# Kernel tuning notes

Measured on AMD Instinct MI355X. Metric: run time of the kernel, lower is better.

## Reference

```python
import jax, jax.numpy as jnp
import numpy as np

B, LG = 16, 128            # graphs, nodes per graph
N = B * LG                 # total nodes
LAT, HID, EE, NL = 32, 128, 32, 3
T_STEPS = 100


def setup_inputs() -> dict:
    key = jax.random.key(0)
    ks = list(jax.random.split(key, 64))
    ki = iter(ks)

    def gl(shape):
        fan_in = shape[-2] if len(shape) >= 2 else shape[-1]
        return jax.random.normal(next(ki), shape, dtype=jnp.float32) / np.sqrt(fan_in)

    # ---- graph structure (mirrors FullDPM._get_edges, done under no_grad) ----
    lengths = np.full((B,), LG, dtype=np.int32)
    batch_ids = np.repeat(np.arange(B, dtype=np.int32), LG)
    chain_ids = np.tile((np.arange(LG) >= LG // 2).astype(np.int32), B)  # 2 chains/graph
    rr, cc = np.meshgrid(np.arange(LG), np.arange(LG), indexing='ij')
    offs = (np.arange(B, dtype=np.int64) * LG)[:, None]
    row = (offs + rr.ravel()[None, :]).ravel()
    col = (offs + cc.ravel()[None, :]).ravel()
    is_ctx = chain_ids[row] == chain_ids[col]
    row2 = np.concatenate([row[is_ctx], row[~is_ctx]])
    col2 = np.concatenate([col[is_ctx], col[~is_ctx]])
    edge_types = np.concatenate([np.zeros(is_ctx.sum(), np.int32),
                                 np.ones((~is_ctx).sum(), np.int32)])
    edges = np.stack([row2, col2], axis=0).astype(np.int32)

    inp = {
        'H_0': jax.random.normal(next(ki), (N, LAT), jnp.float32),
        'X_0': jax.random.normal(next(ki), (N, 3), jnp.float32),
        'cond_embedding': jax.random.normal(next(ki), (N, HID), jnp.float32),
        'eps_H': jax.random.normal(next(ki), (N, LAT), jnp.float32),
        'eps_X': jax.random.normal(next(ki), (N, 3), jnp.float32),
        # params: input_mlp MLP(LAT+2*HID -> HID, 3 layers, ReLU)
        'in_W1': gl((LAT + 2 * HID, HID)), 'in_b1': jnp.zeros((HID,)),
        'in_W2': gl((HID, HID)), 'in_b2': jnp.zeros((HID,)),
        'in_W3': gl((HID, HID)), 'in_b3': jnp.zeros((HID,)),
        'edge_emb': gl((2, EE)),
        'h2i_W': gl((HID, LAT)), 'h2i_b': jnp.zeros((LAT,)),
        # EPT encoder (EGNN-style), NL layers stacked
        'pe_W1': gl((NL, 2 * HID + EE + 1, HID)), 'pe_b1': jnp.zeros((NL, HID)),
        'pe_W2': gl((NL, HID, HID)), 'pe_b2': jnp.zeros((NL, HID)),
        'ph_W1': gl((NL, 2 * HID, HID)), 'ph_b1': jnp.zeros((NL, HID)),
        'ph_W2': gl((NL, HID, HID)), 'ph_b2': jnp.zeros((NL, HID)),
        'px_W': gl((NL, HID, 1)), 'px_b': jnp.zeros((NL, 1)),
        # int / bool inputs
        'generate_mask': jax.random.randint(next(ki), (N,), 0, 2) == 1,
        'batch_ids': jnp.asarray(batch_ids),
        'edges': jnp.asarray(edges),
        'edge_types': jnp.asarray(edge_types),
        'lengths': jnp.asarray(lengths),
        't': jax.random.randint(next(ki), (B,), 0, T_STEPS + 1).astype(jnp.int32),
    }
    return inp


def _time_embed(beta, dim):
    half = dim // 2
    freqs = jnp.exp(-jnp.log(jnp.asarray(10000.0, beta.dtype)) *
                    jnp.arange(half, dtype=beta.dtype) / (half - 1))
    args = beta[:, None] * freqs[None, :]
    return jnp.concatenate([jnp.sin(args), jnp.cos(args)], axis=-1)


def reference(H_0, X_0, cond_embedding, eps_H, eps_X,
              in_W1, in_b1, in_W2, in_b2, in_W3, in_b3,
              edge_emb, h2i_W, h2i_b,
              pe_W1, pe_b1, pe_W2, pe_b2,
              ph_W1, ph_b1, ph_W2, ph_b2, px_W, px_b,
              generate_mask, batch_ids, edges, edge_types, lengths, t):
    n = H_0.shape[0]
    maskf = generate_mask[:, None].astype(H_0.dtype)

    # --- DDPM forward noising (trans_x / trans_h .add_noise) ---
    betas = jnp.linspace(1e-4, 0.02, T_STEPS + 1, dtype=H_0.dtype)
    alpha_bar = jnp.cumprod(1.0 - betas)
    ab = alpha_bar[t][batch_ids][:, None]            # (N,1)
    X_noisy = jnp.where(maskf > 0, jnp.sqrt(ab) * X_0 + jnp.sqrt(1.0 - ab) * eps_X, X_0)
    H_noisy = jnp.where(maskf > 0, jnp.sqrt(ab) * H_0 + jnp.sqrt(1.0 - ab) * eps_H, H_0)
    beta_node = betas[t][batch_ids]                  # (N,)

    # --- EpsilonNet ---
    t_emb = _time_embed(beta_node, HID)
    feat = jnp.concatenate([H_noisy, cond_embedding, t_emb], axis=-1)
    h = jax.nn.relu(feat @ in_W1 + in_b1)
    h = jax.nn.relu(h @ in_W2 + in_b2)
    h = h @ in_W3 + in_b3

    e_feat = edge_emb[edge_types]                    # (E, EE)
    row, col = edges[0], edges[1]
    deg = lengths[batch_ids].astype(H_0.dtype)[:, None]  # full per-graph meshgrid degree
    x = X_noisy
    for l in range(NL):
        dvec = x[row] - x[col]                       # (E,3)
        dist2 = jnp.sum(dvec * dvec, axis=-1, keepdims=True)
        m_in = jnp.concatenate([h[row], h[col], e_feat, dist2], axis=-1)
        m = jax.nn.relu(m_in @ pe_W1[l] + pe_b1[l])
        m = jax.nn.relu(m @ pe_W2[l] + pe_b2[l])     # (E, HID)
        agg = jax.ops.segment_sum(m, row, num_segments=n)
        u = jax.nn.relu(jnp.concatenate([h, agg], axis=-1) @ ph_W1[l] + ph_b1[l])
        h = h + u @ ph_W2[l] + ph_b2[l]
        xm = dvec * (m @ px_W[l] + px_b[l])          # (E,3)
        x = x + jax.ops.segment_sum(xm, row, num_segments=n) / deg

    eps_X_pred = (x - X_noisy) * maskf
    eps_H_pred = ((h @ h2i_W + h2i_b) - H_noisy) * maskf

    # --- masked MSE losses ---
    cnt = jnp.sum(generate_mask).astype(H_0.dtype) + 1e-8
    dX = (eps_X_pred - eps_X) * maskf
    dH = (eps_H_pred - eps_H) * maskf
    loss_X = jnp.sum(dX * dX) / cnt
    loss_H = jnp.sum(dH * dH) / cnt
    return jnp.stack([loss_X, loss_H])
```

## Files before the change

### kernel.cpp

```cpp
#include <hip/hip_runtime.h>
#include <math.h>

#define NN 2048
#define NGRAPH 16
#define LG 128
#define LATD 32
#define HIDD 128

typedef __attribute__((ext_vector_type(8))) short short8;
typedef __attribute__((ext_vector_type(4))) float f32x4;

#define OFF_XN   0
#define OFF_HN   (OFF_XN + NN*3)
#define OFF_W2T  (OFF_HN + NN*LATD)
#define OFF_SAB  (OFF_W2T + 24576)
#define OFF_TB   (OFF_SAB + 32)
#define OFF_H    (OFF_TB + NGRAPH*HIDD)
#define OFF_XA   (OFF_H + NN*HIDD)
#define OFF_XB   (OFF_XA + NN*3)
#define OFF_PR   (OFF_XB + NN*3)
#define OFF_PCE0 (OFF_PR + NN*HIDD)
#define OFF_PCE1 (OFF_PCE0 + NN*HIDD)
#define OFF_ACC  (OFF_PCE1 + NN*HIDD)

__device__ __forceinline__ unsigned short f2bf(float f) {
  unsigned u = __float_as_uint(f);
  u += 0x7fffu + ((u >> 16) & 1u);
  return (unsigned short)(u >> 16);
}

__global__ __launch_bounds__(128) void graph_prep_kernel(
    const int* __restrict__ tarr, const float* __restrict__ inW1,
    const float* __restrict__ inb1,
    float* __restrict__ sab, float* __restrict__ tbias, float* __restrict__ acc)
{
  __shared__ float temb[128];
  int g = blockIdx.x;
  int t = threadIdx.x;
  if (g == 0 && t < 4) acc[t] = 0.f;
  int tt = tarr[g];
  float prod = 1.f;
  for (int i=0; i<=tt; ++i) {
    float beta = 1e-4f + 1.99e-4f*(float)i;
    prod *= (1.f - beta);
  }
  float beta_t = 1e-4f + 1.99e-4f*(float)tt;
  if (t == 0) {
    sab[2*g]   = sqrtf(prod);
    sab[2*g+1] = sqrtf(fmaxf(1.f - prod, 0.f));
  }
  if (t < 64) {
    float freq = __expf(-9.210340371976184f * (float)t / 63.f);
    float arg = beta_t * freq;
    temb[t]      = sinf(arg);
    temb[t + 64] = cosf(arg);
  }
  __syncthreads();
  float s = inb1[t];
  for (int k=0;k<128;++k) s += temb[k] * inW1[(160+k)*HIDD + t];
  tbias[g*HIDD + t] = s;
}

__global__ __launch_bounds__(256) void noise_kernel(
    const float* __restrict__ H0, const float* __restrict__ X0,
    const float* __restrict__ epsH, const float* __restrict__ epsX,
    const int* __restrict__ gmask, const float* __restrict__ sab,
    float* __restrict__ Hn, float* __restrict__ Xn, float* __restrict__ xa)
{
  int idx = blockIdx.x*256 + threadIdx.x;
  if (idx < NN*LATD) {
    int n = idx >> 5;
    int g = n >> 7;
    float sa = sab[2*g], sb = sab[2*g+1];
    float v = H0[idx];
    Hn[idx] = gmask[n] ? sa*v + sb*epsH[idx] : v;
  } else {
    int j = idx - NN*LATD;
    if (j < NN*3) {
      int n = j / 3;
      int g = n >> 7;
      float sa = sab[2*g], sb = sab[2*g+1];
      float v = X0[j];
      float xn = gmask[n] ? sa*v + sb*epsX[j] : v;
      Xn[j] = xn;
      xa[j] = xn;
    }
  }
}

__global__ __launch_bounds__(128) void w2t_kernel(
    const float* __restrict__ peW2, unsigned short* __restrict__ w2t)
{
  int l = blockIdx.x;
  int t = threadIdx.x;
  const float* W = peW2 + (size_t)l*HIDD*HIDD;
  unsigned* dst = (unsigned*)(w2t + (size_t)l*HIDD*HIDD);
  for (int k2=0; k2<64; ++k2) {
    float v0 = W[(2*k2)*HIDD + t];
    float v1 = W[(2*k2+1)*HIDD + t];
    dst[t*64 + k2] = (unsigned)f2bf(v0) | ((unsigned)f2bf(v1) << 16);
  }
}

__global__ __launch_bounds__(256) void node_init_kernel(
    const float* __restrict__ Hn, const float* __restrict__ cond,
    const float* __restrict__ tbias, const float* __restrict__ W1,
    const float* __restrict__ W2, const float* __restrict__ b2,
    const float* __restrict__ W3, const float* __restrict__ b3,
    const float* __restrict__ peW1_0, const float* __restrict__ peb1_0,
    const float* __restrict__ eemb,
    float* __restrict__ h, float* __restrict__ Pr, unsigned short* __restrict__ pce)
{
  __shared__ float fL[4][160];
  __shared__ float pbuf[2][4][HIDD];
  __shared__ float h1[4][HIDD];
  __shared__ float h2[4][HIDD];
  __shared__ float hF[4][HIDD];
  int tt = threadIdx.x;
  int nb = blockIdx.x*4;
  int g = nb >> 7;
  int c = tt & 127, half = tt >> 7;
  for (int idx=tt; idx<4*LATD; idx+=256) {
    int nl = idx>>5, k = idx&31;
    fL[nl][k] = Hn[(size_t)nb*LATD + idx];
  }
  for (int idx=tt; idx<4*HIDD; idx+=256) {
    int nl = idx>>7, k = idx&127;
    fL[nl][32+k] = cond[(size_t)nb*HIDD + idx];
  }
  __syncthreads();
  float p[4];
  #pragma unroll
  for (int nl=0;nl<4;++nl) p[nl]=0.f;
  for (int k=half*80; k<half*80+80; ++k) {
    float w = W1[k*HIDD+c];
    #pragma unroll
    for (int nl=0;nl<4;++nl) p[nl] += fL[nl][k]*w;
  }
  #pragma unroll
  for (int nl=0;nl<4;++nl) pbuf[half][nl][c] = p[nl];
  __syncthreads();
  {
    float tb = tbias[g*HIDD + c];
    #pragma unroll
    for (int q=0;q<2;++q) {
      int nl = half*2+q;
      h1[nl][c] = fmaxf(tb + pbuf[0][nl][c] + pbuf[1][nl][c], 0.f);
    }
  }
  __syncthreads();
  #pragma unroll
  for (int nl=0;nl<4;++nl) p[nl]=0.f;
  for (int k=half*64; k<half*64+64; ++k) {
    float w = W2[k*HIDD+c];
    #pragma unroll
    for (int nl=0;nl<4;++nl) p[nl] += h1[nl][k]*w;
  }
  #pragma unroll
  for (int nl=0;nl<4;++nl) pbuf[half][nl][c] = p[nl];
  __syncthreads();
  #pragma unroll
  for (int q=0;q<2;++q) {
    int nl = half*2+q;
    h2[nl][c] = fmaxf(b2[c] + pbuf[0][nl][c] + pbuf[1][nl][c], 0.f);
  }
  __syncthreads();
  #pragma unroll
  for (int nl=0;nl<4;++nl) p[nl]=0.f;
  for (int k=half*64; k<half*64+64; ++k) {
    float w = W3[k*HIDD+c];
    #pragma unroll
    for (int nl=0;nl<4;++nl) p[nl] += h2[nl][k]*w;
  }
  #pragma unroll
  for (int nl=0;nl<4;++nl) pbuf[half][nl][c] = p[nl];
  __syncthreads();
  #pragma unroll
  for (int q=0;q<2;++q) {
    int nl = half*2+q;
    float v = b3[c] + pbuf[0][nl][c] + pbuf[1][nl][c];
    hF[nl][c] = v;
    h[(size_t)(nb+nl)*HIDD+c] = v;
  }
  __syncthreads();
  const float* W = peW1_0 + half*HIDD*HIDD;
  float a[4];
  #pragma unroll
  for (int nl=0;nl<4;++nl) a[nl]=0.f;
  for (int k=0;k<HIDD;++k) {
    float w = W[k*HIDD+c];
    #pragma unroll
    for (int nl=0;nl<4;++nl) a[nl] += hF[nl][k]*w;
  }
  if (half == 0) {
    #pragma unroll
    for (int nl=0;nl<4;++nl) Pr[(size_t)(nb+nl)*HIDD+c] = a[nl];
  } else {
    float e0 = peb1_0[c], e1 = peb1_0[c];
    for (int k=0;k<32;++k) {
      float w = peW1_0[(256+k)*HIDD+c];
      e0 += eemb[k]*w;
      e1 += eemb[32+k]*w;
    }
    #pragma unroll
    for (int nl=0;nl<4;++nl) {
      pce[((size_t)(nb+nl))*HIDD + c]      = f2bf(a[nl] + e0);
      pce[((size_t)(NN + nb+nl))*HIDD + c] = f2bf(a[nl] + e1);
    }
  }
}

__device__ __forceinline__ short8 buildA(uint4 p, f32x4 prA, f32x4 prB,
                                         f32x4 wdA, f32x4 wdB, float d2) {
  float s[8];
  unsigned pu[4] = {p.x, p.y, p.z, p.w};
  #pragma unroll
  for (int q=0;q<4;++q) {
    float lo = __uint_as_float(pu[q] << 16);
    float hi = __uint_as_float(pu[q] & 0xffff0000u);
    float pr0 = (q<2) ? prA[2*q]   : prB[2*q-4];
    float pr1 = (q<2) ? prA[2*q+1] : prB[2*q-3];
    float wd0 = (q<2) ? wdA[2*q]   : wdB[2*q-4];
    float wd1 = (q<2) ? wdA[2*q+1] : wdB[2*q-3];
    s[2*q]   = fmaxf(pr0 + lo + d2*wd0, 0.f);
    s[2*q+1] = fmaxf(pr1 + hi + d2*wd1, 0.f);
  }
  uint4 r;
  asm("v_cvt_pk_bf16_f32 %0, %1, %2" : "=v"(r.x) : "v"(s[0]), "v"(s[1]));
  asm("v_cvt_pk_bf16_f32 %0, %1, %2" : "=v"(r.y) : "v"(s[2]), "v"(s[3]));
  asm("v_cvt_pk_bf16_f32 %0, %1, %2" : "=v"(r.z) : "v"(s[4]), "v"(s[5]));
  asm("v_cvt_pk_bf16_f32 %0, %1, %2" : "=v"(r.w) : "v"(s[6]), "v"(s[7]));
  return *(short8*)&r;
}

template<bool NEXT>
__global__ __launch_bounds__(256, 3) void layer_kernel(
    const float* __restrict__ xR, float* __restrict__ xW,
    float* __restrict__ Pr,
    const unsigned short* __restrict__ pceR, unsigned short* __restrict__ pceW,
    const unsigned short* __restrict__ w2t,
    const float* __restrict__ peW1l, const float* __restrict__ peb2l,
    const float* __restrict__ pxWl, const float* __restrict__ pxbl,
    float* __restrict__ hbuf,
    const float* __restrict__ phW1l, const float* __restrict__ phb1l,
    const float* __restrict__ phW2l, const float* __restrict__ phb2l,
    const float* __restrict__ peW1n, const float* __restrict__ peb1n,
    const float* __restrict__ eemb, const int* __restrict__ lengths)
{
  __shared__ __align__(16) unsigned short W2s[HIDD*HIDD];
  __shared__ __align__(16) float PrL[HIDD];
  __shared__ __align__(16) float W1dL[HIDD];
  __shared__ float b2L[HIDD];
  __shared__ float pxWL[HIDD];
  __shared__ float d2L[LG];
  __shared__ float dvL[LG][3];
  __shared__ float xgL[LG][3];
  __shared__ float SxL[3];
  __shared__ float aggAll[4][HIDD];
  __shared__ float xmAll[4][3];
  __shared__ float hL[4][HIDD];
  __shared__ float uL[4][HIDD];
  __shared__ float hN[4][HIDD];
  __shared__ float partU[2][4][HIDD];
  __shared__ float EFbL[2][HIDD];

  int tt = threadIdx.x;
  int bid = blockIdx.x;
  int g = bid >> 5, ib = bid & 31;
  int i0 = ib*4;
  int nbase = g*LG;

  {
    int col = tt & 127, kh = tt >> 7;
    const uint4* src = (const uint4*)(w2t + (size_t)col*HIDD + kh*64);
    #pragma unroll
    for (int c8=0;c8<8;++c8) {
      uint4 v = src[c8];
      int koff2 = (kh*64 + c8*8)*2;
      int byteoff = col*256 + (koff2 ^ ((col&7)<<4));
      *(uint4*)((char*)W2s + byteoff) = v;
    }
  }
  if (tt < HIDD) {
    W1dL[tt] = peW1l[288*HIDD + tt];
    b2L[tt]  = peb2l[tt];
    pxWL[tt] = pxWl[tt];
  }
  for (int idx=tt; idx<LG*3; idx+=256)
    ((float*)xgL)[idx] = xR[(size_t)nbase*3 + idx];
  __syncthreads();
  if (tt < 3) {
    float s = 0.f;
    for (int j=0;j<LG;++j) s += xgL[j][tt];
    SxL[tt] = s;
  }
  float pxb0 = pxbl[0];

  int w = tt >> 6, l = tt & 63;
  int l15 = l & 15, lg2 = l >> 4;
  int wrow = w * 32;
  int j0 = wrow + l15, j1 = j0 + 16;

  for (int ii=0; ii<4; ++ii) {
    int i = i0 + ii;
    __syncthreads();
    if (tt < LG) {
      int j = tt;
      float dx = xgL[i][0]-xgL[j][0];
      float dy = xgL[i][1]-xgL[j][1];
      float dz = xgL[i][2]-xgL[j][2];
      dvL[j][0]=dx; dvL[j][1]=dy; dvL[j][2]=dz;
      d2L[j] = dx*dx+dy*dy+dz*dz;
      aggAll[ii][j] = 0.f;
    } else {
      PrL[tt-128] = Pr[(size_t)(nbase+i)*HIDD + (tt-128)];
    }
    if (tt >= 252 && tt < 255) xmAll[ii][tt-252] = 0.f;
    __syncthreads();

    int ci = (i >= 64) ? 1 : 0;
    int et0 = (ci != ((j0 >= 64) ? 1 : 0)) ? 1 : 0;
    int et1 = (ci != ((j1 >= 64) ? 1 : 0)) ? 1 : 0;
    const unsigned short* pceB0 = pceR + ((size_t)(et0*NN + nbase + j0))*HIDD;
    const unsigned short* pceB1 = pceR + ((size_t)(et1*NN + nbase + j1))*HIDD;
    float d2a = d2L[j0], d2b = d2L[j1];

    f32x4 zz = {0.f,0.f,0.f,0.f};
    f32x4 acc[2][8];
    #pragma unroll
    for (int r=0;r<2;++r)
      #pragma unroll
      for (int cf=0;cf<8;++cf) acc[r][cf] = zz;

    #pragma unroll
    for (int kk=0;kk<4;++kk) {
      int ks = kk*32 + lg2*8;
      f32x4 prA = *(const f32x4*)&PrL[ks];
      f32x4 prB = *(const f32x4*)&PrL[ks+4];
      f32x4 wdA = *(const f32x4*)&W1dL[ks];
      f32x4 wdB = *(const f32x4*)&W1dL[ks+4];
      uint4 pa = *(const uint4*)(pceB0 + ks);
      uint4 pb = *(const uint4*)(pceB1 + ks);
      short8 a0 = buildA(pa, prA, prB, wdA, wdB, d2a);
      short8 a1 = buildA(pb, prA, prB, wdA, wdB, d2b);
      int kbyte = kk*64 + lg2*16;
      #pragma unroll
      for (int cf=0;cf<8;++cf) {
        int col = cf*16 + l15;
        int boff = col*256 + (kbyte ^ ((col&7)<<4));
        short8 bF = *(const short8*)((const char*)W2s + boff);
        acc[0][cf] = __builtin_amdgcn_mfma_f32_16x16x32_bf16(a0, bF, acc[0][cf], 0,0,0);
        acc[1][cf] = __builtin_amdgcn_mfma_f32_16x16x32_bf16(a1, bF, acc[1][cf], 0,0,0);
      }
    }

    float pxp[2][4];
    #pragma unroll
    for (int r=0;r<2;++r)
      #pragma unroll
      for (int q=0;q<4;++q) pxp[r][q] = 0.f;
    #pragma unroll
    for (int cf=0;cf<8;++cf) {
      int col = cf*16 + l15;
      float b2v = b2L[col], pxv = pxWL[col];
      float aggp = 0.f;
      #pragma unroll
      for (int r=0;r<2;++r)
        #pragma unroll
        for (int q=0;q<4;++q) {
          float m = fmaxf(acc[r][cf][q] + b2v, 0.f);
          aggp += m;
          pxp[r][q] += m * pxv;
        }
      aggp += __shfl_xor(aggp, 16);
      aggp += __shfl_xor(aggp, 32);
      if (l < 16) atomicAdd(&aggAll[ii][col], aggp);
    }
    float xmx=0.f, xmy=0.f, xmz=0.f;
    #pragma unroll
    for (int r=0;r<2;++r)
      #pragma unroll
      for (int q=0;q<4;++q) {
        int j = wrow + r*16 + lg2*4 + q;
        float p = pxp[r][q];
        xmx += p*dvL[j][0]; xmy += p*dvL[j][1]; xmz += p*dvL[j][2];
      }
    #pragma unroll
    for (int s=1; s<64; s<<=1) {
      xmx += __shfl_xor(xmx, s);
      xmy += __shfl_xor(xmy, s);
      xmz += __shfl_xor(xmz, s);
    }
    if (l == 0) {
      atomicAdd(&xmAll[ii][0], xmx);
      atomicAdd(&xmAll[ii][1], xmy);
      atomicAdd(&xmAll[ii][2], xmz);
    }
  }

  int c = tt & 127, half = tt >> 7;
  for (int idx=tt; idx<4*HIDD; idx+=256)
    ((float*)hL)[idx] = hbuf[(size_t)(nbase+i0)*HIDD + idx];
  if (NEXT) {
    int e = half;
    float s = peb1n[c];
    for (int k=0;k<32;++k) s += eemb[e*32+k]*peW1n[(256+k)*HIDD+c];
    EFbL[e][c] = s;
  }
  __syncthreads();

  float p[4];
  {
    const float (*cat)[HIDD] = half ? aggAll : hL;
    #pragma unroll
    for (int nl=0;nl<4;++nl) p[nl]=0.f;
    const float* Wb = phW1l + (size_t)(half*HIDD)*HIDD + c;
    for (int k=0;k<HIDD;++k) {
      float wv = Wb[k*HIDD];
      #pragma unroll
      for (int nl=0;nl<4;++nl) p[nl] += cat[nl][k]*wv;
    }
    #pragma unroll
    for (int nl=0;nl<4;++nl) partU[half][nl][c] = p[nl];
  }
  __syncthreads();
  #pragma unroll
  for (int q=0;q<2;++q) {
    int nl = half*2+q;
    uL[nl][c] = fmaxf(phb1l[c] + partU[0][nl][c] + partU[1][nl][c], 0.f);
  }
  __syncthreads();
  {
    #pragma unroll
    for (int nl=0;nl<4;++nl) p[nl]=0.f;
    const float* Wb = phW2l + (size_t)(half*64)*HIDD + c;
    for (int k=0;k<64;++k) {
      float wv = Wb[k*HIDD];
      #pragma unroll
      for (int nl=0;nl<4;++nl) p[nl] += uL[nl][half*64+k]*wv;
    }
    #pragma unroll
    for (int nl=0;nl<4;++nl) partU[half][nl][c] = p[nl];
  }
  __syncthreads();
  #pragma unroll
  for (int q=0;q<2;++q) {
    int nl = half*2+q;
    float hn = hL[nl][c] + phb2l[c] + partU[0][nl][c] + partU[1][nl][c];
    hN[nl][c] = hn;
    hbuf[(size_t)(nbase+i0+nl)*HIDD+c] = hn;
  }
  __syncthreads();
  if (NEXT) {
    const float* W = peW1n + (size_t)half*HIDD*HIDD;
    float a[4];
    #pragma unroll
    for (int nl=0;nl<4;++nl) a[nl]=0.f;
    for (int k=0;k<HIDD;++k) {
      float wv = W[k*HIDD+c];
      #pragma unroll
      for (int nl=0;nl<4;++nl) a[nl] += hN[nl][k]*wv;
    }
    if (half == 0) {
      #pragma unroll
      for (int nl=0;nl<4;++nl) Pr[(size_t)(nbase+i0+nl)*HIDD+c] = a[nl];
    } else {
      float e0 = EFbL[0][c], e1 = EFbL[1][c];
      #pragma unroll
      for (int nl=0;nl<4;++nl) {
        pceW[((size_t)(nbase+i0+nl))*HIDD + c]      = f2bf(a[nl] + e0);
        pceW[((size_t)(NN + nbase+i0+nl))*HIDD + c] = f2bf(a[nl] + e1);
      }
    }
  }
  if (tt < 12) {
    int nl = tt/3, cc = tt%3;
    int i = i0 + nl;
    float deg = (float)lengths[g];
    float xmv = xmAll[nl][cc] + pxb0*(128.f*xgL[i][cc] - SxL[cc]);
    xW[(size_t)(nbase+i)*3 + cc] = xgL[i][cc] + xmv/deg;
  }
}

__global__ __launch_bounds__(256) void loss_kernel(
    const float* __restrict__ h, const float* __restrict__ h2iW,
    const float* __restrict__ h2ib, const float* __restrict__ Hn,
    const float* __restrict__ Xn, const float* __restrict__ xf,
    const float* __restrict__ epsH, const float* __restrict__ epsX,
    const int* __restrict__ gmask, float* __restrict__ acc)
{
  __shared__ float hL[8][HIDD];
  __shared__ float rX[256], rH[256], rC[256];
  int tt = threadIdx.x;
  int nb = blockIdx.x*8;
  for (int idx=tt; idx<8*HIDD; idx+=256)
    ((float*)hL)[idx] = h[(size_t)nb*HIDD + idx];
  __syncthreads();
  int nl = tt>>5, c = tt&31;
  int n = nb+nl;
  float mf = gmask[n] ? 1.f : 0.f;
  float pj = h2ib[c];
  for (int k=0;k<HIDD;++k) pj += hL[nl][k]*h2iW[k*LATD+c];
  float dH = mf*((pj - Hn[n*LATD+c]) - epsH[n*LATD+c]);
  float sH = dH*dH;
  float sX = 0.f, sc = 0.f;
  if (c < 3) {
    float dX = mf*((xf[n*3+c]-Xn[n*3+c]) - epsX[n*3+c]);
    sX = dX*dX;
  }
  if (c == 0) sc = mf;
  rX[tt]=sX; rH[tt]=sH; rC[tt]=sc;
  __syncthreads();
  for (int s=128; s>0; s>>=1) {
    if (tt<s) { rX[tt]+=rX[tt+s]; rH[tt]+=rH[tt+s]; rC[tt]+=rC[tt+s]; }
    __syncthreads();
  }
  if (tt==0) {
    atomicAdd(&acc[0], rX[0]);
    atomicAdd(&acc[1], rH[0]);
    atomicAdd(&acc[2], rC[0]);
  }
}

__global__ void finalize_kernel(const float* __restrict__ acc, float* __restrict__ out) {
  if (threadIdx.x==0) {
    float cnt = acc[2] + 1e-8f;
    out[0] = acc[0]/cnt;
    out[1] = acc[1]/cnt;
  }
}

extern "C" void kernel_launch(void* const* d_in, const int* in_sizes, int n_in,
                              void* d_out, int out_size, void* d_ws, size_t ws_size,
                              hipStream_t stream) {
  (void)in_sizes; (void)n_in; (void)out_size; (void)ws_size;
  const float* H0    = (const float*)d_in[0];
  const float* X0    = (const float*)d_in[1];
  const float* cond  = (const float*)d_in[2];
  const float* epsH  = (const float*)d_in[3];
  const float* epsX  = (const float*)d_in[4];
  const float* inW1  = (const float*)d_in[5];
  const float* inb1  = (const float*)d_in[6];
  const float* inW2  = (const float*)d_in[7];
  const float* inb2  = (const float*)d_in[8];
  const float* inW3  = (const float*)d_in[9];
  const float* inb3  = (const float*)d_in[10];
  const float* eemb  = (const float*)d_in[11];
  const float* h2iW  = (const float*)d_in[12];
  const float* h2ib  = (const float*)d_in[13];
  const float* peW1  = (const float*)d_in[14];
  const float* peb1  = (const float*)d_in[15];
  const float* peW2  = (const float*)d_in[16];
  const float* peb2  = (const float*)d_in[17];
  const float* phW1  = (const float*)d_in[18];
  const float* phb1  = (const float*)d_in[19];
  const float* phW2  = (const float*)d_in[20];
  const float* phb2  = (const float*)d_in[21];
  const float* pxW   = (const float*)d_in[22];
  const float* pxB   = (const float*)d_in[23];
  const int* gmask   = (const int*)d_in[24];
  const int* batch   = (const int*)d_in[25];
  (void)batch;
  const int* lengths = (const int*)d_in[28];
  const int* tarr    = (const int*)d_in[29];

  float* ws  = (float*)d_ws;
  float* out = (float*)d_out;
  float* Xn   = ws + OFF_XN;
  float* Hn   = ws + OFF_HN;
  unsigned short* w2tb = (unsigned short*)(ws + OFF_W2T);
  float* sabb = ws + OFF_SAB;
  float* tbb  = ws + OFF_TB;
  float* hbuf = ws + OFF_H;
  float* Xa   = ws + OFF_XA;
  float* Xb   = ws + OFF_XB;
  float* Prb  = ws + OFF_PR;
  unsigned short* pce0 = (unsigned short*)(ws + OFF_PCE0);
  unsigned short* pce1 = (unsigned short*)(ws + OFF_PCE1);
  float* accb = ws + OFF_ACC;

  graph_prep_kernel<<<NGRAPH, 128, 0, stream>>>(tarr, inW1, inb1, sabb, tbb, accb);
  noise_kernel<<<(NN*LATD + NN*3 + 255)/256, 256, 0, stream>>>(
      H0, X0, epsH, epsX, gmask, sabb, Hn, Xn, Xa);
  w2t_kernel<<<3, 128, 0, stream>>>(peW2, w2tb);
  node_init_kernel<<<NN/4, 256, 0, stream>>>(
      Hn, cond, tbb, inW1, inW2, inb2, inW3, inb3,
      peW1, peb1, eemb, hbuf, Prb, pce0);

  layer_kernel<true><<<NGRAPH*32, 256, 0, stream>>>(
      Xa, Xb, Prb, pce0, pce1, w2tb + 0*(size_t)HIDD*HIDD,
      peW1 + 0*(size_t)289*HIDD, peb2 + 0*HIDD, pxW + 0*HIDD, pxB + 0,
      hbuf, phW1 + 0*(size_t)256*HIDD, phb1 + 0*HIDD,
      phW2 + 0*(size_t)HIDD*HIDD, phb2 + 0*HIDD,
      peW1 + 1*(size_t)289*HIDD, peb1 + 1*HIDD, eemb, lengths);
  layer_kernel<true><<<NGRAPH*32, 256, 0, stream>>>(
      Xb, Xa, Prb, pce1, pce0, w2tb + 1*(size_t)HIDD*HIDD,
      peW1 + 1*(size_t)289*HIDD, peb2 + 1*HIDD, pxW + 1*HIDD, pxB + 1,
      hbuf, phW1 + 1*(size_t)256*HIDD, phb1 + 1*HIDD,
      phW2 + 1*(size_t)HIDD*HIDD, phb2 + 1*HIDD,
      peW1 + 2*(size_t)289*HIDD, peb1 + 2*HIDD, eemb, lengths);
  layer_kernel<false><<<NGRAPH*32, 256, 0, stream>>>(
      Xa, Xb, Prb, pce0, nullptr, w2tb + 2*(size_t)HIDD*HIDD,
      peW1 + 2*(size_t)289*HIDD, peb2 + 2*HIDD, pxW + 2*HIDD, pxB + 2,
      hbuf, phW1 + 2*(size_t)256*HIDD, phb1 + 2*HIDD,
      phW2 + 2*(size_t)HIDD*HIDD, phb2 + 2*HIDD,
      nullptr, nullptr, eemb, lengths);

  loss_kernel<<<NN/8, 256, 0, stream>>>(hbuf, h2iW, h2ib, Hn, Xn, Xb,
                                        epsH, epsX, gmask, accb);
  finalize_kernel<<<1, 64, 0, stream>>>(accb, out);
}
```

Before: 278.5 us.

## Assign one source node per wave in EGNN layer kernel, removing per-node barriers

The edge-message loop used to process the block's four source nodes one after another, with all four waves splitting the 128 neighbours and two block barriers per node plus shared-memory atomics for the aggregation. Now each wave owns one source node and walks all 128 neighbours in four chunks. Distances are computed in registers and column sums are kept per lane, so the inner barriers, the atomics and the dvL/d2L staging go away. The A fragments are also built up front before the MFMA loop. The cost is more registers per wave (colsum, a0/a1 arrays), which could lower occupancy under the 3-blocks launch bound.

```diff
diff --git a/kernel.cpp b/kernel.cpp
--- a/kernel.cpp
+++ b/kernel.cpp
@@ -248,12 +248,10 @@
     const float* __restrict__ eemb, const int* __restrict__ lengths)
 {
   __shared__ __align__(16) unsigned short W2s[HIDD*HIDD];
-  __shared__ __align__(16) float PrL[HIDD];
+  __shared__ __align__(16) float PrL[4][HIDD];
   __shared__ __align__(16) float W1dL[HIDD];
   __shared__ float b2L[HIDD];
   __shared__ float pxWL[HIDD];
-  __shared__ float d2L[LG];
-  __shared__ float dvL[LG][3];
   __shared__ float xgL[LG][3];
   __shared__ float SxL[3];
   __shared__ float aggAll[4][HIDD];
@@ -270,6 +268,10 @@
   int i0 = ib*4;
   int nbase = g*LG;
 
+  int w = tt >> 6, l = tt & 63;
+  int l15 = l & 15, lg2 = l >> 4;
+  int i = i0 + w;
+
   {
     int col = tt & 127, kh = tt >> 7;
     const uint4* src = (const uint4*)(w2t + (size_t)col*HIDD + kh*64);
@@ -288,6 +290,8 @@
   }
   for (int idx=tt; idx<LG*3; idx+=256)
     ((float*)xgL)[idx] = xR[(size_t)nbase*3 + idx];
+  for (int idx=l; idx<HIDD; idx+=64)
+    PrL[w][idx] = Pr[(size_t)(nbase+i)*HIDD + idx];
   __syncthreads();
   if (tt < 3) {
     float s = 0.f;
@@ -296,61 +300,55 @@
   }
   float pxb0 = pxbl[0];
 
-  int w = tt >> 6, l = tt & 63;
-  int l15 = l & 15, lg2 = l >> 4;
-  int wrow = w * 32;
-  int j0 = wrow + l15, j1 = j0 + 16;
-
-  for (int ii=0; ii<4; ++ii) {
-    int i = i0 + ii;
-    __syncthreads();
-    if (tt < LG) {
-      int j = tt;
-      float dx = xgL[i][0]-xgL[j][0];
-      float dy = xgL[i][1]-xgL[j][1];
-      float dz = xgL[i][2]-xgL[j][2];
-      dvL[j][0]=dx; dvL[j][1]=dy; dvL[j][2]=dz;
-      d2L[j] = dx*dx+dy*dy+dz*dz;
-      aggAll[ii][j] = 0.f;
-    } else {
-      PrL[tt-128] = Pr[(size_t)(nbase+i)*HIDD + (tt-128)];
-    }
-    if (tt >= 252 && tt < 255) xmAll[ii][tt-252] = 0.f;
-    __syncthreads();
-
-    int ci = (i >= 64) ? 1 : 0;
+  float xi0 = xgL[i][0], xi1 = xgL[i][1], xi2 = xgL[i][2];
+  int ci = (i >= 64) ? 1 : 0;
+  float colsum[8];
+  #pragma unroll
+  for (int cf=0;cf<8;++cf) colsum[cf] = 0.f;
+  float xmx = 0.f, xmy = 0.f, xmz = 0.f;
+
+  for (int jp=0; jp<4; ++jp) {
+    int j0 = jp*32 + l15, j1 = j0 + 16;
+    float dxa = xi0 - xgL[j0][0], dya = xi1 - xgL[j0][1], dza = xi2 - xgL[j0][2];
+    float d2a = dxa*dxa + dya*dya + dza*dza;
+    float dxb = xi0 - xgL[j1][0], dyb = xi1 - xgL[j1][1], dzb = xi2 - xgL[j1][2];
+    float d2b = dxb*dxb + dyb*dyb + dzb*dzb;
     int et0 = (ci != ((j0 >= 64) ? 1 : 0)) ? 1 : 0;
     int et1 = (ci != ((j1 >= 64) ? 1 : 0)) ? 1 : 0;
     const unsigned short* pceB0 = pceR + ((size_t)(et0*NN + nbase + j0))*HIDD;
     const unsigned short* pceB1 = pceR + ((size_t)(et1*NN + nbase + j1))*HIDD;
-    float d2a = d2L[j0], d2b = d2L[j1];
-
-    f32x4 zz = {0.f,0.f,0.f,0.f};
-    f32x4 acc[2][8];
-    #pragma unroll
-    for (int r=0;r<2;++r)
-      #pragma unroll
-      for (int cf=0;cf<8;++cf) acc[r][cf] = zz;
-
+
+    short8 a0[4], a1[4];
     #pragma unroll
     for (int kk=0;kk<4;++kk) {
       int ks = kk*32 + lg2*8;
-      f32x4 prA = *(const f32x4*)&PrL[ks];
-      f32x4 prB = *(const f32x4*)&PrL[ks+4];
+      f32x4 prA = *(const f32x4*)&PrL[w][ks];
+      f32x4 prB = *(const f32x4*)&PrL[w][ks+4];
       f32x4 wdA = *(const f32x4*)&W1dL[ks];
       f32x4 wdB = *(const f32x4*)&W1dL[ks+4];
       uint4 pa = *(const uint4*)(pceB0 + ks);
       uint4 pb = *(const uint4*)(pceB1 + ks);
-      short8 a0 = buildA(pa, prA, prB, wdA, wdB, d2a);
-      short8 a1 = buildA(pb, prA, prB, wdA, wdB, d2b);
+      a0[kk] = buildA(pa, prA, prB, wdA, wdB, d2a);
+      a1[kk] = buildA(pb, prA, prB, wdA, wdB, d2b);
+    }
+
+    f32x4 zz = {0.f,0.f,0.f,0.f};
+    f32x4 acc[2][8];
+    #pragma unroll
+    for (int r=0;r<2;++r)
+      #pragma unroll
+      for (int cf=0;cf<8;++cf) acc[r][cf] = zz;
+
+    #pragma unroll
+    for (int kk=0;kk<4;++kk) {
       int kbyte = kk*64 + lg2*16;
       #pragma unroll
       for (int cf=0;cf<8;++cf) {
         int col = cf*16 + l15;
         int boff = col*256 + (kbyte ^ ((col&7)<<4));
         short8 bF = *(const short8*)((const char*)W2s + boff);
-        acc[0][cf] = __builtin_amdgcn_mfma_f32_16x16x32_bf16(a0, bF, acc[0][cf], 0,0,0);
-        acc[1][cf] = __builtin_amdgcn_mfma_f32_16x16x32_bf16(a1, bF, acc[1][cf], 0,0,0);
+        acc[0][cf] = __builtin_amdgcn_mfma_f32_16x16x32_bf16(a0[kk], bF, acc[0][cf], 0,0,0);
+        acc[1][cf] = __builtin_amdgcn_mfma_f32_16x16x32_bf16(a1[kk], bF, acc[1][cf], 0,0,0);
       }
     }
 
@@ -363,40 +361,41 @@
     for (int cf=0;cf<8;++cf) {
       int col = cf*16 + l15;
       float b2v = b2L[col], pxv = pxWL[col];
-      float aggp = 0.f;
       #pragma unroll
       for (int r=0;r<2;++r)
         #pragma unroll
         for (int q=0;q<4;++q) {
           float m = fmaxf(acc[r][cf][q] + b2v, 0.f);
-          aggp += m;
+          colsum[cf] += m;
           pxp[r][q] += m * pxv;
         }
-      aggp += __shfl_xor(aggp, 16);
-      aggp += __shfl_xor(aggp, 32);
-      if (l < 16) atomicAdd(&aggAll[ii][col], aggp);
-    }
-    float xmx=0.f, xmy=0.f, xmz=0.f;
+    }
     #pragma unroll
     for (int r=0;r<2;++r)
       #pragma unroll
       for (int q=0;q<4;++q) {
-        int j = wrow + r*16 + lg2*4 + q;
+        int row = jp*32 + r*16 + lg2*4 + q;
         float p = pxp[r][q];
-        xmx += p*dvL[j][0]; xmy += p*dvL[j][1]; xmz += p*dvL[j][2];
+        xmx += p*(xi0 - xgL[row][0]);
+        xmy += p*(xi1 - xgL[row][1]);
+        xmz += p*(xi2 - xgL[row][2]);
       }
-    #pragma unroll
-    for (int s=1; s<64; s<<=1) {
-      xmx += __shfl_xor(xmx, s);
-      xmy += __shfl_xor(xmy, s);
-      xmz += __shfl_xor(xmz, s);
-    }
-    if (l == 0) {
-      atomicAdd(&xmAll[ii][0], xmx);
-      atomicAdd(&xmAll[ii][1], xmy);
-      atomicAdd(&xmAll[ii][2], xmz);
-    }
-  }
+  }
+
+  #pragma unroll
+  for (int cf=0;cf<8;++cf) {
+    float v = colsum[cf];
+    v += __shfl_xor(v, 16);
+    v += __shfl_xor(v, 32);
+    if (l < 16) aggAll[w][cf*16 + l15] = v;
+  }
+  #pragma unroll
+  for (int s=1; s<64; s<<=1) {
+    xmx += __shfl_xor(xmx, s);
+    xmy += __shfl_xor(xmy, s);
+    xmz += __shfl_xor(xmz, s);
+  }
+  if (l == 0) { xmAll[w][0] = xmx; xmAll[w][1] = xmy; xmAll[w][2] = xmz; }
 
   int c = tt & 127, half = tt >> 7;
   for (int idx=tt; idx<4*HIDD; idx+=256)
@@ -475,10 +474,10 @@
   }
   if (tt < 12) {
     int nl = tt/3, cc = tt%3;
-    int i = i0 + nl;
+    int ii = i0 + nl;
     float deg = (float)lengths[g];
-    float xmv = xmAll[nl][cc] + pxb0*(128.f*xgL[i][cc] - SxL[cc]);
-    xW[(size_t)(nbase+i)*3 + cc] = xgL[i][cc] + xmv/deg;
+    float xmv = xmAll[nl][cc] + pxb0*(128.f*xgL[ii][cc] - SxL[cc]);
+    xW[(size_t)(nbase+ii)*3 + cc] = xgL[ii][cc] + xmv/deg;
   }
 }
 
```

Result: faster. 259.6 us (-6.8%).
